# Performance work log

Hardware: AMD Instinct MI355X
Metric: run time of the kernel (lower is better)

The kernel has to match this reference:

```python
import jax, jax.numpy as jnp
import numpy as np

H = 12          # num_attention_heads
HD = 64         # head_dim
GAMMA = 0.5
LOCAL_EPS = 0.8
N_APPROX = 7


def _l1norm(x, axis):
    # torch.nn.functional.normalize(x, p=1, dim=axis)
    n = jnp.sum(jnp.abs(x), axis=axis, keepdims=True)
    return x / jnp.maximum(n, 1e-12)


def setup_inputs() -> dict:
    key = jax.random.key(0)
    ks = jax.random.split(key, 6)
    B, S, E = 2, 512, 768
    std = 1.0 / np.sqrt(E)
    hidden_states = jax.random.normal(ks[0], (B, S, E), jnp.float32)
    Wq = jax.random.normal(ks[1], (E, E), jnp.float32) * std
    Wk = jax.random.normal(ks[2], (E, E), jnp.float32) * std
    Wv = jax.random.normal(ks[3], (E, E), jnp.float32) * std
    bq = jnp.zeros((E,), jnp.float32)
    bk = jnp.zeros((E,), jnp.float32)
    bv = jnp.zeros((E,), jnp.float32)
    g = jax.random.randint(ks[4], (B * S, B * S), 0, 2, jnp.int32)
    attention_mask = jnp.zeros((B, S), jnp.float32)
    return {"hidden_states": hidden_states, "Wq": Wq, "bq": bq, "Wk": Wk,
            "bk": bk, "Wv": Wv, "bv": bv, "g": g,
            "attention_mask": attention_mask}


def reference(hidden_states, Wq, bq, Wk, bk, Wv, bv, g, attention_mask):
    B, S, E = hidden_states.shape
    BN = B * S
    x = hidden_states  # torch flattens batch-major: token index = b*S + s
    q = (x @ Wq + bq) / jnp.sqrt(jnp.float32(HD))
    k = x @ Wk + bk
    v = x @ Wv + bv
    # [B,S,E] -> [BN,H,HD] -> [H,BN,HD]
    q = q.reshape(BN, H, HD).transpose(1, 0, 2)
    k = k.reshape(BN, H, HD).transpose(1, 0, 2)
    v = v.reshape(BN, H, HD).transpose(1, 0, 2)

    # W_G[h,i,j] = exp(k_i . q_j)
    W_G = jnp.exp(jnp.einsum('hid,hjd->hij', k, q))

    # sparsification mask combined with token mask
    bool_mask = (attention_mask >= 0).reshape(-1).astype(jnp.int32)  # [BN]
    g_eff = g * (bool_mask[:, None] * bool_mask[None, :])
    W_G = jnp.where(g_eff > 0, W_G, jnp.zeros((), W_G.dtype))

    out_degree = W_G.sum(axis=2)                       # [H, BN]
    rhos = jax.lax.stop_gradient(out_degree.max(axis=1))  # [H]

    eye = jnp.eye(BN, dtype=W_G.dtype)
    Bmat = rhos[:, None, None] * eye + W_G - out_degree[:, :, None] * eye

    B_power = jnp.broadcast_to(eye, (H, BN, BN))
    L_gamma = jnp.broadcast_to(eye, (H, BN, BN))
    num = 1.0
    den = jnp.ones((H,), W_G.dtype)
    for ii in range(1, N_APPROX + 1):  # fixed 7-term power series
        num = num * (GAMMA - ii + 1) * -1.0
        den = den * (ii * rhos)
        coef = num / den                               # [H]
        B_power = jnp.einsum('hij,hjk->hik', Bmat, B_power)
        L_gamma = L_gamma + coef[:, None, None] * B_power
    L_gamma = L_gamma * (rhos[:, None, None] ** GAMMA)
    diags = jnp.diagonal(L_gamma, axis1=-2, axis2=-1)  # [H, BN]
    L_gamma = _l1norm(diags[:, :, None] * eye - L_gamma, axis=2)

    attn = (LOCAL_EPS * jnp.einsum('hij,hjd->hid', _l1norm(W_G, 2), v)
            + (1.0 - LOCAL_EPS) * jnp.einsum('hij,hjd->hid', L_gamma, v))

    # faithful to torch: raw reshape of [H,BN,HD] into [B,S,H,HD]
    out = attn.reshape(B, S, H, HD)
    out = jnp.swapaxes(out, 0, 1).reshape(S, B, E)
    return jnp.swapaxes(out, 0, 1)
```

## Files before the change

kernel.cpp:

```cpp
#include <hip/hip_runtime.h>
#include <hip/hip_bf16.h>

typedef __attribute__((ext_vector_type(4))) float f32x4;
typedef __attribute__((ext_vector_type(8))) short s16x8;

typedef const __attribute__((address_space(1))) void* gptr_t;
typedef __attribute__((address_space(3))) void* lptr_t;

__device__ __forceinline__ short f2b(float f){ __hip_bfloat16 h=__float2bfloat16(f); return *(short*)&h; }
__device__ __forceinline__ float b2f(short s){ __hip_bfloat16 h; *(short*)&h = s; return __bfloat162float(h); }

__device__ __forceinline__ void gl_lds16(const void* g, void* l){
  __builtin_amdgcn_global_load_lds((gptr_t)g, (lptr_t)l, 16, 0, 0);
}


__global__ __launch_bounds__(256) void cvt_x(const float* __restrict__ X, short* __restrict__ Xb){
  int i = blockIdx.x*256 + threadIdx.x;
  const float4* p = (const float4*)(X + (size_t)i*8);
  float4 a = p[0], b = p[1];
  s16x8 o;
  o[0]=f2b(a.x); o[1]=f2b(a.y); o[2]=f2b(a.z); o[3]=f2b(a.w);
  o[4]=f2b(b.x); o[5]=f2b(b.y); o[6]=f2b(b.z); o[7]=f2b(b.w);
  *(s16x8*)(Xb + (size_t)i*8) = o;
}

__global__ __launch_bounds__(256) void cvt_wt(const float* __restrict__ W, short* __restrict__ WT){
  __shared__ short tile[64][72];
  int bl = blockIdx.x % 12, bn = blockIdx.x / 12;
  int l0 = bl*64, n0 = bn*64;
  int t = threadIdx.x;
  #pragma unroll
  for (int p=0;p<4;p++){
    int lr = p*16 + (t>>4);
    int nc = (t&15)*4;
    float4 v = *(const float4*)(W + (size_t)(l0+lr)*768 + n0 + nc);
    tile[lr][nc+0]=f2b(v.x); tile[lr][nc+1]=f2b(v.y); tile[lr][nc+2]=f2b(v.z); tile[lr][nc+3]=f2b(v.w);
  }
  __syncthreads();
  #pragma unroll
  for (int p=0;p<2;p++){
    int nr = p*32 + (t>>3);
    int lc = (t&7)*8;
    s16x8 o;
    #pragma unroll
    for(int u=0;u<8;u++) o[u] = tile[lc+u][nr];
    *(s16x8*)(WT + (size_t)(n0+nr)*768 + l0 + lc) = o;
  }
}

__global__ void bmask_k(const float* __restrict__ am, float* __restrict__ bmf){
  int i = blockIdx.x*256+threadIdx.x;
  if (i<1024) bmf[i] = (am[i] >= 0.0f) ? 1.0f : 0.0f;
}

__global__ __launch_bounds__(256) void vtrans(const short* __restrict__ vs, short* __restrict__ vT){
  __shared__ short tile[64][72];
  int h = blockIdx.y; int i0 = blockIdx.x*64;
  int t = threadIdx.x;
  #pragma unroll
  for(int p=0;p<2;p++){
    int ir = p*32 + (t>>3); int c8=(t&7)*8;
    *(s16x8*)&tile[ir][c8] = *(const s16x8*)(vs + (size_t)(i0+ir)*768 + h*64 + c8);
  }
  __syncthreads();
  #pragma unroll
  for(int p=0;p<2;p++){
    int dr = p*32 + (t>>3); int i8=(t&7)*8;
    s16x8 o;
    #pragma unroll
    for(int u=0;u<8;u++) o[u]=tile[i8+u][dr];
    *(s16x8*)(vT + ((size_t)h*64 + dr)*1024 + i0 + i8) = o;
  }
}

__global__ __launch_bounds__(256) void qkv_gemm(const short* __restrict__ Xb, const short* __restrict__ WT,
      const float* __restrict__ bq, const float* __restrict__ bk, const float* __restrict__ bv,
      short* __restrict__ qs, short* __restrict__ ks, short* __restrict__ vs){
  __shared__ short lA[128*32], lB[128*32];
  int mat = blockIdx.y;
  const short* B = WT + (size_t)mat*768*768;
  const float* bias = mat==0?bq:(mat==1?bk:bv);
  short* outp = mat==0?qs:(mat==1?ks:vs);
  float scale = mat==0 ? 0.125f : 1.0f;
  int tm = (blockIdx.x / 6)*128, tn = (blockIdx.x % 6)*128;
  int t=threadIdx.x, wave=t>>6, lane=t&63;
  int srow=t>>2, scol=(t&3)*8;
  int wm=(wave>>1)*64, wn=(wave&1)*64;
  f32x4 acc[4][4]={};
  for (int k0=0;k0<768;k0+=32){
    #pragma unroll
    for(int r=0;r<2;++r){
      gl_lds16(Xb + (size_t)(tm+srow+r*64)*768 + k0 + scol, lA + r*2048 + wave*512);
      gl_lds16(B  + (size_t)(tn+srow+r*64)*768 + k0 + scol, lB + r*2048 + wave*512);
    }
    __syncthreads();
    int krow=(lane>>4)*8, rl=lane&15;
    s16x8 af[4], bfr[4];
    #pragma unroll
    for(int m=0;m<4;m++) af[m] = *(s16x8*)&lA[(wm+m*16+rl)*32 + krow];
    #pragma unroll
    for(int n=0;n<4;n++) bfr[n] = *(s16x8*)&lB[(wn+n*16+rl)*32 + krow];
    #pragma unroll
    for(int m=0;m<4;m++)
      #pragma unroll
      for(int n=0;n<4;n++)
        acc[m][n]=__builtin_amdgcn_mfma_f32_16x16x32_bf16(af[m],bfr[n],acc[m][n],0,0,0);
    __syncthreads();
  }
  int r0 = tm + wm + (lane>>4)*4, c0 = tn + wn + (lane&15);
  #pragma unroll
  for(int m=0;m<4;m++)
    #pragma unroll
    for(int n=0;n<4;n++){
      int col = c0 + n*16; float bb = bias[col];
      #pragma unroll
      for(int r=0;r<4;r++){
        int row = r0 + m*16 + r;
        outp[(size_t)row*768 + col] = f2b((acc[m][n][r] + bb)*scale);
      }
    }
}

__global__ __launch_bounds__(256) void wg_gemm(const short* __restrict__ kb, const short* __restrict__ qb,
      const int* __restrict__ g, const float* __restrict__ bmf,
      short* __restrict__ WG, float* __restrict__ od){
  __shared__ short lK[128*64], lQ[128*64];
  int h=blockIdx.y;
  int tm=(blockIdx.x>>3)*128, tn=(blockIdx.x&7)*128;
  int t=threadIdx.x, wave=t>>6, lane=t&63;
  int srow=t>>3, scol=(t&7)*8;
  int wm=(wave>>1)*64, wn=(wave&1)*64;
  #pragma unroll
  for(int r=0;r<4;++r){
    gl_lds16(kb + (size_t)(tm+srow+r*32)*768 + h*64 + scol, lK + r*2048 + wave*512);
    gl_lds16(qb + (size_t)(tn+srow+r*32)*768 + h*64 + scol, lQ + r*2048 + wave*512);
  }
  __syncthreads();
  int rl=lane&15;
  f32x4 acc[4][4]={};
  #pragma unroll
  for(int ks=0;ks<2;ks++){
    int krow=ks*32+(lane>>4)*8;
    s16x8 af[4], bfr[4];
    #pragma unroll
    for(int m=0;m<4;m++) af[m]=*(s16x8*)&lK[(wm+m*16+rl)*64+krow];
    #pragma unroll
    for(int n=0;n<4;n++) bfr[n]=*(s16x8*)&lQ[(wn+n*16+rl)*64+krow];
    #pragma unroll
    for(int m=0;m<4;m++)
      #pragma unroll
      for(int n=0;n<4;n++)
        acc[m][n]=__builtin_amdgcn_mfma_f32_16x16x32_bf16(af[m],bfr[n],acc[m][n],0,0,0);
  }
  size_t hm=(size_t)h<<20;
  int r0=tm+wm+(lane>>4)*4, c0=tn+wn+rl;
  #pragma unroll
  for(int m=0;m<4;m++){
    float rs[4]={0.f,0.f,0.f,0.f};
    #pragma unroll
    for(int n=0;n<4;n++){
      int col=c0+n*16;
      float mc = bmf[col];
      #pragma unroll
      for(int r=0;r<4;r++){
        int row=r0+m*16+r;
        float e = expf(acc[m][n][r]);
        float w = (g[(size_t)row*1024+col]>0 && bmf[row]>0.f && mc>0.f) ? e : 0.f;
        WG[hm+(size_t)row*1024+col]=f2b(w);
        rs[r]+=w;
      }
    }
    #pragma unroll
    for(int r=0;r<4;r++){
      float s=rs[r];
      #pragma unroll
      for(int off=1;off<16;off<<=1) s+=__shfl_xor(s,off);
      if(rl==0) atomicAdd(&od[(h<<10)+r0+m*16+r], s);
    }
  }
}

__global__ void rhos_k(const float* __restrict__ od, float* __restrict__ rhos){
  __shared__ float red[256];
  int h = blockIdx.x, t = threadIdx.x;
  float m = -1e30f;
  for (int i=t;i<1024;i+=256) m = fmaxf(m, od[(h<<10)+i]);
  red[t]=m; __syncthreads();
  for(int s=128;s>0;s>>=1){ if(t<s) red[t]=fmaxf(red[t],red[t+s]); __syncthreads(); }
  if(t==0) rhos[h]=red[0];
}

__global__ __launch_bounds__(256) void amat_t(const short* __restrict__ WG, const float* __restrict__ od,
      const float* __restrict__ rhos, short* __restrict__ Am, short* __restrict__ AmT,
      short* __restrict__ T){
  __shared__ short tile[64][72];
  const float b7 = -33.f/2048.f, b6 = -21.f/1024.f;
  int h = blockIdx.y; int bx = blockIdx.x;
  int rb = bx >> 4, cb = bx & 15;
  int r0 = rb*64, c0 = cb*64;
  float rho = rhos[h]; float inv = 1.0f/fmaxf(rho,1e-30f);
  size_t hm = (size_t)h<<20;
  int t = threadIdx.x;
  #pragma unroll
  for(int p=0;p<2;p++){
    int r = p*32 + (t>>3); int c8 = (t&7)*8;
    size_t base = hm + (size_t)(r0+r)*1024 + c0 + c8;
    s16x8 w = *(const s16x8*)(WG + base);
    s16x8 oa, ot;
    float dadd = (rho - od[(h<<10)+r0+r])*inv;
    #pragma unroll
    for(int u=0;u<8;u++){
      bool dg = (rb==cb) && ((c8+u)==r);
      float a = b2f(w[u])*inv + (dg ? dadd : 0.f);
      oa[u]=f2b(a);
      ot[u]=f2b(b7*a + (dg ? b6 : 0.f));
      tile[r][c8+u]=oa[u];
    }
    *(s16x8*)(Am+base)=oa; *(s16x8*)(T+base)=ot;
  }
  __syncthreads();
  #pragma unroll
  for(int p=0;p<2;p++){
    int c = p*32 + (t>>3); int r8 = (t&7)*8;
    s16x8 o;
    #pragma unroll
    for(int u=0;u<8;u++) o[u]=tile[r8+u][c];
    *(s16x8*)(AmT + hm + (size_t)(c0+c)*1024 + r0 + r8) = o;
  }
}

template<int EPI, bool STAT>
__global__ __launch_bounds__(256) void gemm_ps(const short* __restrict__ A, const short* __restrict__ B,
      short* __restrict__ D, const short* __restrict__ E1, const short* __restrict__ E2,
      float c0c, float cA, float cB, float* __restrict__ rowabs, float* __restrict__ dvp){
  __shared__ short lA[128*32], lB[128*32];
  int h=blockIdx.y;
  int tm=(blockIdx.x>>3)*128, tn=(blockIdx.x&7)*128;
  size_t hm=(size_t)h<<20;
  int t=threadIdx.x, wave=t>>6, lane=t&63;
  int srow=t>>2, scol=(t&3)*8;
  int wm=(wave>>1)*64, wn=(wave&1)*64;
  f32x4 acc[4][4]={};
  for(int k0=0;k0<1024;k0+=32){
    #pragma unroll
    for(int r=0;r<2;++r){
      gl_lds16(A + hm + (size_t)(tm+srow+r*64)*1024 + k0 + scol, lA + r*2048 + wave*512);
      gl_lds16(B + hm + (size_t)(tn+srow+r*64)*1024 + k0 + scol, lB + r*2048 + wave*512);
    }
    __syncthreads();
    int krow=(lane>>4)*8, rl=lane&15;
    s16x8 af[4], bfr[4];
    #pragma unroll
    for(int m=0;m<4;m++) af[m]=*(s16x8*)&lA[(wm+m*16+rl)*32+krow];
    #pragma unroll
    for(int n=0;n<4;n++) bfr[n]=*(s16x8*)&lB[(wn+n*16+rl)*32+krow];
    #pragma unroll
    for(int m=0;m<4;m++)
      #pragma unroll
      for(int n=0;n<4;n++)
        acc[m][n]=__builtin_amdgcn_mfma_f32_16x16x32_bf16(af[m],bfr[n],acc[m][n],0,0,0);
    __syncthreads();
  }
  int r0=tm+wm+(lane>>4)*4, c0=tn+wn+(lane&15);
  int rl=lane&15;
  #pragma unroll
  for(int m=0;m<4;m++){
    float rs[4]={0.f,0.f,0.f,0.f};
    #pragma unroll
    for(int n=0;n<4;n++){
      int col=c0+n*16;
      #pragma unroll
      for(int r=0;r<4;r++){
        int row=r0+m*16+r;
        float v=acc[m][n][r];
        if (EPI==1){
          size_t e = hm + (size_t)row*1024 + col;
          v += cA*b2f(E1[e]) + cB*b2f(E2[e]);
          if(row==col) v += c0c;
        }
        if (STAT){
          rs[r] += fabsf(v);
          if(row==col) dvp[(h<<10)+row] = v;
        }
        D[hm + (size_t)row*1024 + col]=f2b(v);
      }
    }
    if (STAT){
      #pragma unroll
      for(int r=0;r<4;r++){
        float s=rs[r];
        #pragma unroll
        for(int off=1;off<16;off<<=1) s+=__shfl_xor(s,off);
        if(rl==0) atomicAdd(&rowabs[(h<<10)+r0+m*16+r], s);
      }
    }
  }
}

__global__ __launch_bounds__(256) void attn_k(const short* __restrict__ WG, const short* __restrict__ L,
    const short* __restrict__ vT, const short* __restrict__ vs,
    const float* __restrict__ od, const float* __restrict__ dv, const float* __restrict__ rowabs,
    float* __restrict__ out){
  __shared__ short lW[128*32], lL[128*32], lV[64*32];
  int h=blockIdx.y, tm=blockIdx.x*128;
  size_t hm=(size_t)h<<20;
  int t=threadIdx.x, wave=t>>6, lane=t&63;
  int srow=t>>2, scol=(t&3)*8;
  f32x4 a1[2][4]={}, a2[2][4]={};
  for(int j0=0;j0<1024;j0+=32){
    #pragma unroll
    for(int r=0;r<2;++r){
      gl_lds16(WG + hm + (size_t)(tm+srow+r*64)*1024 + j0 + scol, lW + r*2048 + wave*512);
      gl_lds16(L  + hm + (size_t)(tm+srow+r*64)*1024 + j0 + scol, lL + r*2048 + wave*512);
    }
    gl_lds16(vT + ((size_t)h*64 + srow)*1024 + j0 + scol, lV + wave*512);
    __syncthreads();
    int krow=(lane>>4)*8, rl=lane&15;
    s16x8 fw[2], fl[2], fv[4];
    #pragma unroll
    for(int m=0;m<2;m++){
      fw[m]=*(s16x8*)&lW[(wave*32+m*16+rl)*32+krow];
      fl[m]=*(s16x8*)&lL[(wave*32+m*16+rl)*32+krow];
    }
    #pragma unroll
    for(int n=0;n<4;n++) fv[n]=*(s16x8*)&lV[(n*16+rl)*32+krow];
    #pragma unroll
    for(int m=0;m<2;m++)
      #pragma unroll
      for(int n=0;n<4;n++){
        a1[m][n]=__builtin_amdgcn_mfma_f32_16x16x32_bf16(fw[m],fv[n],a1[m][n],0,0,0);
        a2[m][n]=__builtin_amdgcn_mfma_f32_16x16x32_bf16(fl[m],fv[n],a2[m][n],0,0,0);
      }
    __syncthreads();
  }
  #pragma unroll
  for(int m=0;m<2;m++)
    #pragma unroll
    for(int r=0;r<4;r++){
      int row = tm + wave*32 + m*16 + (lane>>4)*4 + r;
      float invod = 1.0f/fmaxf(od[(h<<10)+row], 1e-12f);
      float dvi = dv[(h<<10)+row];
      float ivr = 1.0f/fmaxf(rowabs[(h<<10)+row] - fabsf(dvi), 1e-12f);
      #pragma unroll
      for(int n=0;n<4;n++){
        int d = n*16 + (lane&15);
        float vv = b2f(vs[(size_t)row*768 + h*64 + d]);
        out[(((size_t)h<<10)+row)*64 + d] = 0.8f*a1[m][n][r]*invod + 0.2f*(dvi*vv - a2[m][n][r])*ivr;
      }
    }
}

extern "C" void kernel_launch(void* const* d_in, const int* in_sizes, int n_in,
                              void* d_out, int out_size, void* d_ws, size_t ws_size,
                              hipStream_t stream){
  const float* hs = (const float*)d_in[0];
  const float* Wq = (const float*)d_in[1];
  const float* bq = (const float*)d_in[2];
  const float* Wk = (const float*)d_in[3];
  const float* bk = (const float*)d_in[4];
  const float* Wv = (const float*)d_in[5];
  const float* bv = (const float*)d_in[6];
  const int*   g  = (const int*)d_in[7];
  const float* am = (const float*)d_in[8];
  float* out = (float*)d_out;

  char* w = (char*)d_ws;
  auto alloc=[&](size_t bytes)->char*{ char* p=w; w += (bytes+255)&~(size_t)255; return p; };
  short* Xb  = (short*)alloc((size_t)1024*768*2);
  short* WT  = (short*)alloc((size_t)3*768*768*2);
  short* qs  = (short*)alloc((size_t)1024*768*2);
  short* ks  = (short*)alloc((size_t)1024*768*2);
  short* vs  = (short*)alloc((size_t)1024*768*2);
  short* vT  = (short*)alloc((size_t)12*64*1024*2);
  short* WG  = (short*)alloc((size_t)12*1024*1024*2);
  short* Am  = (short*)alloc((size_t)12*1024*1024*2);
  short* AmT = (short*)alloc((size_t)12*1024*1024*2);
  short* Tm  = (short*)alloc((size_t)12*1024*1024*2);
  short* A2  = (short*)alloc((size_t)12*1024*1024*2);
  short* A3T = (short*)alloc((size_t)12*1024*1024*2);
  float* od  = (float*)alloc((size_t)12*1024*4);
  float* rh  = (float*)alloc((size_t)64*4);
  float* bmf = (float*)alloc((size_t)1024*4);
  float* dv  = (float*)alloc((size_t)12*1024*4);
  float* rab = (float*)alloc((size_t)12*1024*4);

  hipMemsetAsync(od,  0, (size_t)12*1024*4, stream);
  hipMemsetAsync(rab, 0, (size_t)12*1024*4, stream);

  cvt_x<<<384,256,0,stream>>>(hs, Xb);
  cvt_wt<<<144,256,0,stream>>>(Wq, WT);
  cvt_wt<<<144,256,0,stream>>>(Wk, WT + (size_t)768*768);
  cvt_wt<<<144,256,0,stream>>>(Wv, WT + (size_t)2*768*768);
  bmask_k<<<4,256,0,stream>>>(am, bmf);
  qkv_gemm<<<dim3(48,3),256,0,stream>>>(Xb, WT, bq,bk,bv, qs,ks,vs);
  vtrans<<<dim3(16,12),256,0,stream>>>(vs, vT);
  wg_gemm<<<dim3(64,12),256,0,stream>>>(ks, qs, g, bmf, WG, od);
  rhos_k<<<12,256,0,stream>>>(od, rh);
  amat_t<<<dim3(256,12),256,0,stream>>>(WG, od, rh, Am, AmT, Tm);

  const float b1=-0.5f, b2=-0.125f, b3=-1.f/16.f, b4=-5.f/128.f, b5=-7.f/256.f;
  short* V = AmT;
  short* L = Tm;
  gemm_ps<0,false><<<dim3(64,12),256,0,stream>>>(Am, AmT, A2, nullptr,nullptr, 0,0,0, nullptr,nullptr);
  gemm_ps<0,false><<<dim3(64,12),256,0,stream>>>(AmT, A2, A3T, nullptr,nullptr, 0,0,0, nullptr,nullptr);
  gemm_ps<1,false><<<dim3(64,12),256,0,stream>>>(Tm, A3T, V, Am, A2, b3,b4,b5, nullptr,nullptr);
  gemm_ps<1,true><<<dim3(64,12),256,0,stream>>>(V, A3T, L, Am, A2, 1.0f,b1,b2, rab, dv);

  attn_k<<<dim3(8,12),256,0,stream>>>(WG, L, vT, vs, od, dv, rab, out);
}
```

Measured before the change: 318.8 us.

## Rewrite power-series GEMMs as 256x256 double-buffered 8-wave pipelined kernels

Replaces the 128x128 single-buffered batched GEMM used for the four power-series matrix products with a 256x256-tile, 512-thread kernel. It double-buffers LDS with direct global-to-LDS loads issued one phase ahead, XOR-swizzles LDS to avoid bank conflicts, and uses explicit waitcnt, barriers and setprio to overlap MFMA with loads. It also remaps workgroups across the 192-block grid. This targets the memory-bound small-tile loop, at the cost of 128KB of LDS per block, high register pressure and fragile hand-written synchronization.

```diff
diff --git a/kernel.cpp b/kernel.cpp
--- a/kernel.cpp
+++ b/kernel.cpp
@@ -230,70 +230,155 @@
   }
 }
 
-template<int EPI, bool STAT>
-__global__ __launch_bounds__(256) void gemm_ps(const short* __restrict__ A, const short* __restrict__ B,
+
+#define PH(MH, KS, D_, DOST, U, KT, DN, WN) { \
+  if (DOST) { \
+    _Pragma("unroll") \
+    for (int r_=0;r_<2;r_++){ \
+      const short* sp_ = ((U)<2 ? Ag : Bg) + (size_t)(((U)<2 ? tm : tn) + rS[r_])*1024 + (KT)*64 + ((U)&1)*32 + cS[r_]; \
+      gl_lds16(sp_, &lds[DN][U][r_*4096 + wave*512]); \
+    } \
+  } \
+  const char* au_ = (const char*)&lds[D_][KS][0]; \
+  const char* bu_ = (const char*)&lds[D_][2+(KS)][0]; \
+  s16x8 af_[4], bf_[4]; \
+  _Pragma("unroll") \
+  for (int m_=0;m_<4;m_++) af_[m_] = *(const s16x8*)(au_ + aoff[MH][m_]); \
+  _Pragma("unroll") \
+  for (int n_=0;n_<4;n_++) bf_[n_] = *(const s16x8*)(bu_ + boff[n_]); \
+  __builtin_amdgcn_s_barrier(); \
+  asm volatile("s_waitcnt lgkmcnt(0)" ::: "memory"); \
+  __builtin_amdgcn_sched_barrier(0); \
+  __builtin_amdgcn_s_setprio(1); \
+  _Pragma("unroll") \
+  for (int m_=0;m_<4;m_++) \
+    _Pragma("unroll") \
+    for (int n_=0;n_<4;n_++) \
+      acc[(MH)*4+m_][n_] = __builtin_amdgcn_mfma_f32_16x16x32_bf16(af_[m_], bf_[n_], acc[(MH)*4+m_][n_], 0,0,0); \
+  __builtin_amdgcn_s_setprio(0); \
+  if ((WN)==4) { asm volatile("s_waitcnt vmcnt(4)" ::: "memory"); } \
+  else if ((WN)==0) { asm volatile("s_waitcnt vmcnt(0)" ::: "memory"); } \
+  __builtin_amdgcn_s_barrier(); }
+
+#define GEMM8P_PROLOG \
+  __shared__ short lds[2][4][8192]; \
+  int wg = ((int)blockIdx.x & 7)*24 + ((int)blockIdx.x >> 3); \
+  int h = wg >> 4; int tile_ = wg & 15; \
+  int tm = (tile_>>2)*256, tn = (tile_&3)*256; \
+  size_t hm = (size_t)h<<20; \
+  const short* Ag = A + hm; const short* Bg = B + hm; \
+  int tid = threadIdx.x, wave = tid>>6, lane = tid&63; \
+  int wm = wave>>2, wn = wave&3; \
+  int rl = lane & 15; \
+  int rS[2], cS[2]; \
+  _Pragma("unroll") \
+  for (int r_=0;r_<2;r_++){ \
+    int alpha = (r_*512 + tid)*16; int row = alpha>>6; int q = (row ^ (row>>2)) & 3; \
+    rS[r_] = row; cS[r_] = (((alpha&63) ^ (q<<4))>>1); \
+  } \
+  int aoff[2][4], boff[4]; \
+  { int koff = ((lane>>4)&3)*16; \
+    _Pragma("unroll") \
+    for (int mh_=0;mh_<2;mh_++) \
+      _Pragma("unroll") \
+      for (int m_=0;m_<4;m_++){ int rho = wm*128 + mh_*64 + m_*16 + rl; int lin = rho*64 + koff; \
+        aoff[mh_][m_] = lin ^ (((rho^(rho>>2))&3)<<4); } \
+    _Pragma("unroll") \
+    for (int n_=0;n_<4;n_++){ int rho = wn*64 + n_*16 + rl; int lin = rho*64 + koff; \
+      boff[n_] = lin ^ (((rho^(rho>>2))&3)<<4); } \
+  } \
+  f32x4 acc[8][4] = {}; \
+   \
+  _Pragma("unroll") \
+  for (int u_=0;u_<4;u_++){ \
+    _Pragma("unroll") \
+    for (int r_=0;r_<2;r_++){ \
+      const short* sp_ = (u_<2 ? Ag : Bg) + (size_t)((u_<2 ? tm : tn) + rS[r_])*1024 + (u_&1)*32 + cS[r_]; \
+      gl_lds16(sp_, &lds[0][u_][r_*4096 + wave*512]); \
+    } \
+  } \
+  asm volatile("s_waitcnt vmcnt(4)" ::: "memory"); \
+  __builtin_amdgcn_s_barrier(); \
+  _Pragma("unroll 1") \
+  for (int t_=0; t_<15; ++t_){ \
+    const int d_ = t_&1, dn_ = d_^1; \
+    PH(0,0, d_, 1, 0, t_+1, dn_, -1) \
+    PH(1,0, d_, 1, 1, t_+1, dn_, 4) \
+    PH(0,1, d_, 1, 2, t_+1, dn_, -1) \
+    PH(1,1, d_, 1, 3, t_+1, dn_, 4) \
+  } \
+  PH(0,0, 1, 0, 0, 0, 0, -1) \
+  PH(1,0, 1, 0, 0, 0, 0, 0) \
+  PH(0,1, 1, 0, 0, 0, 0, -1) \
+  PH(1,1, 1, 0, 0, 0, 0, -1) \
+  int rb = tm + wm*128 + ((lane>>4)&3)*4; \
+  int cb = tn + wn*64 + rl;
+
+__global__ __launch_bounds__(512,2) void gemm8p_plain(const short* __restrict__ A, const short* __restrict__ B,
+      short* __restrict__ D){
+  GEMM8P_PROLOG
+  short* Dg = D + hm;
+  #pragma unroll
+  for (int f=0;f<8;f++)
+    #pragma unroll
+    for (int n=0;n<4;n++){
+      int col = cb + n*16;
+      #pragma unroll
+      for (int rr=0;rr<4;rr++)
+        Dg[(size_t)(rb + f*16 + rr)*1024 + col] = f2b(acc[f][n][rr]);
+    }
+}
+
+__global__ __launch_bounds__(512,2) void gemm8p_epi(const short* __restrict__ A, const short* __restrict__ B,
+      short* __restrict__ D, const short* __restrict__ E1, const short* __restrict__ E2,
+      float c0c, float cA, float cB){
+  GEMM8P_PROLOG
+  short* Dg = D + hm;
+  const short* E1g = E1 + hm; const short* E2g = E2 + hm;
+  #pragma unroll
+  for (int f=0;f<8;f++)
+    #pragma unroll
+    for (int n=0;n<4;n++){
+      int col = cb + n*16;
+      #pragma unroll
+      for (int rr=0;rr<4;rr++){
+        int row = rb + f*16 + rr;
+        size_t e = (size_t)row*1024 + col;
+        float v = acc[f][n][rr] + cA*b2f(E1g[e]) + cB*b2f(E2g[e]);
+        if (row==col) v += c0c;
+        Dg[e] = f2b(v);
+      }
+    }
+}
+
+__global__ __launch_bounds__(512,2) void gemm8p_epi_stat(const short* __restrict__ A, const short* __restrict__ B,
       short* __restrict__ D, const short* __restrict__ E1, const short* __restrict__ E2,
       float c0c, float cA, float cB, float* __restrict__ rowabs, float* __restrict__ dvp){
-  __shared__ short lA[128*32], lB[128*32];
-  int h=blockIdx.y;
-  int tm=(blockIdx.x>>3)*128, tn=(blockIdx.x&7)*128;
-  size_t hm=(size_t)h<<20;
-  int t=threadIdx.x, wave=t>>6, lane=t&63;
-  int srow=t>>2, scol=(t&3)*8;
-  int wm=(wave>>1)*64, wn=(wave&1)*64;
-  f32x4 acc[4][4]={};
-  for(int k0=0;k0<1024;k0+=32){
-    #pragma unroll
-    for(int r=0;r<2;++r){
-      gl_lds16(A + hm + (size_t)(tm+srow+r*64)*1024 + k0 + scol, lA + r*2048 + wave*512);
-      gl_lds16(B + hm + (size_t)(tn+srow+r*64)*1024 + k0 + scol, lB + r*2048 + wave*512);
-    }
-    __syncthreads();
-    int krow=(lane>>4)*8, rl=lane&15;
-    s16x8 af[4], bfr[4];
-    #pragma unroll
-    for(int m=0;m<4;m++) af[m]=*(s16x8*)&lA[(wm+m*16+rl)*32+krow];
-    #pragma unroll
-    for(int n=0;n<4;n++) bfr[n]=*(s16x8*)&lB[(wn+n*16+rl)*32+krow];
-    #pragma unroll
-    for(int m=0;m<4;m++)
-      #pragma unroll
-      for(int n=0;n<4;n++)
-        acc[m][n]=__builtin_amdgcn_mfma_f32_16x16x32_bf16(af[m],bfr[n],acc[m][n],0,0,0);
-    __syncthreads();
-  }
-  int r0=tm+wm+(lane>>4)*4, c0=tn+wn+(lane&15);
-  int rl=lane&15;
-  #pragma unroll
-  for(int m=0;m<4;m++){
+  GEMM8P_PROLOG
+  short* Dg = D + hm;
+  const short* E1g = E1 + hm; const short* E2g = E2 + hm;
+  #pragma unroll
+  for (int f=0;f<8;f++){
     float rs[4]={0.f,0.f,0.f,0.f};
     #pragma unroll
-    for(int n=0;n<4;n++){
-      int col=c0+n*16;
-      #pragma unroll
-      for(int r=0;r<4;r++){
-        int row=r0+m*16+r;
-        float v=acc[m][n][r];
-        if (EPI==1){
-          size_t e = hm + (size_t)row*1024 + col;
-          v += cA*b2f(E1[e]) + cB*b2f(E2[e]);
-          if(row==col) v += c0c;
-        }
-        if (STAT){
-          rs[r] += fabsf(v);
-          if(row==col) dvp[(h<<10)+row] = v;
-        }
-        D[hm + (size_t)row*1024 + col]=f2b(v);
-      }
-    }
-    if (STAT){
-      #pragma unroll
-      for(int r=0;r<4;r++){
-        float s=rs[r];
-        #pragma unroll
-        for(int off=1;off<16;off<<=1) s+=__shfl_xor(s,off);
-        if(rl==0) atomicAdd(&rowabs[(h<<10)+r0+m*16+r], s);
-      }
+    for (int n=0;n<4;n++){
+      int col = cb + n*16;
+      #pragma unroll
+      for (int rr=0;rr<4;rr++){
+        int row = rb + f*16 + rr;
+        size_t e = (size_t)row*1024 + col;
+        float v = acc[f][n][rr] + cA*b2f(E1g[e]) + cB*b2f(E2g[e]);
+        if (row==col){ v += c0c; dvp[(h<<10)+row] = v; }
+        rs[rr] += fabsf(v);
+        Dg[e] = f2b(v);
+      }
+    }
+    #pragma unroll
+    for (int rr=0;rr<4;rr++){
+      float s=rs[rr];
+      #pragma unroll
+      for(int off=1;off<16;off<<=1) s+=__shfl_xor(s,off);
+      if(rl==0) atomicAdd(&rowabs[(h<<10)+rb+f*16+rr], s);
     }
   }
 }
@@ -402,10 +487,10 @@
   const float b1=-0.5f, b2=-0.125f, b3=-1.f/16.f, b4=-5.f/128.f, b5=-7.f/256.f;
   short* V = AmT;
   short* L = Tm;
-  gemm_ps<0,false><<<dim3(64,12),256,0,stream>>>(Am, AmT, A2, nullptr,nullptr, 0,0,0, nullptr,nullptr);
-  gemm_ps<0,false><<<dim3(64,12),256,0,stream>>>(AmT, A2, A3T, nullptr,nullptr, 0,0,0, nullptr,nullptr);
-  gemm_ps<1,false><<<dim3(64,12),256,0,stream>>>(Tm, A3T, V, Am, A2, b3,b4,b5, nullptr,nullptr);
-  gemm_ps<1,true><<<dim3(64,12),256,0,stream>>>(V, A3T, L, Am, A2, 1.0f,b1,b2, rab, dv);
+  gemm8p_plain<<<192,512,0,stream>>>(Am, AmT, A2);
+  gemm8p_plain<<<192,512,0,stream>>>(AmT, A2, A3T);
+  gemm8p_epi<<<192,512,0,stream>>>(Tm, A3T, V, Am, A2, b3,b4,b5);
+  gemm8p_epi_stat<<<192,512,0,stream>>>(V, A3T, L, Am, A2, 1.0f,b1,b2, rab, dv);
 
   attn_k<<<dim3(8,12),256,0,stream>>>(WG, L, vT, vs, od, dv, rab, out);
 }
```

New measurement: 292.9 us. -8.1%, faster.
